# Performance work log

Hardware: AMD Instinct MI355X
Metric: run time of the kernel (lower is better)

## Reference

```python
import jax, jax.numpy as jnp
import numpy as np
from jax import lax

B, N, C = 256, 256, 192
HEADS = 6
HD = C // HEADS
WIN = 16
AGENT = 49
POOL = 7            # int(agent_num ** 0.5)
SCALE = HD ** -0.5


def _pool_matrix(inn, out):
    # PyTorch AdaptiveAvgPool2d bin edges: start=floor(i*inn/out), end=ceil((i+1)*inn/out)
    P = np.zeros((out, inn), np.float32)
    for i in range(out):
        s = (i * inn) // out
        e = -(((-(i + 1)) * inn) // out)
        P[i, s:e] = 1.0 / (e - s)
    return jnp.asarray(P)

_P = _pool_matrix(WIN, POOL)  # (7, 16) adaptive-avg-pool operator


def _resize_bilinear(x, out_h, out_w):
    # matches F.interpolate(mode='bilinear', align_corners=False)
    H, W = x.shape[-2], x.shape[-1]
    def idx(out, inn):
        s = (jnp.arange(out, dtype=jnp.float32) + 0.5) * (inn / out) - 0.5
        s = jnp.maximum(s, 0.0)
        i0 = jnp.minimum(jnp.floor(s).astype(jnp.int32), inn - 1)
        i1 = jnp.minimum(i0 + 1, inn - 1)
        return i0, i1, s - i0.astype(jnp.float32)
    h0, h1, th = idx(out_h, H)
    w0, w1, tw = idx(out_w, W)
    xh = x[..., h0, :] * (1.0 - th)[:, None] + x[..., h1, :] * th[:, None]
    return xh[..., :, w0] * (1.0 - tw) + xh[..., :, w1] * tw


def setup_inputs() -> dict:
    key = jax.random.key(0)
    ks = jax.random.split(key, 18)
    lin = lambda k: jax.random.normal(k, (C, C), jnp.float32) * 0.02
    zc = jnp.zeros((C,), jnp.float32)
    tn = lambda k, shp: jax.random.normal(k, shp, jnp.float32) * 0.02
    return {
        "x_F1": jax.random.normal(ks[0], (B, N, C), jnp.float32),
        "x_C2": jax.random.normal(ks[1], (B, N, C), jnp.float32),
        "x_C1": jax.random.normal(ks[2], (B, N, C), jnp.float32),
        "Wq": lin(ks[3]), "bq": zc,
        "Wk": lin(ks[4]), "bk": zc,
        "Wv": lin(ks[5]), "bv": zc,
        "Wa1": lin(ks[6]), "ba1": zc,
        "Wa2": lin(ks[7]), "ba2": zc,
        "an_bias": tn(ks[8], (HEADS, AGENT, 7, 7)),
        "na_bias": tn(ks[9], (HEADS, AGENT, 7, 7)),
        "ah_bias": tn(ks[10], (1, HEADS, AGENT, WIN, 1)),
        "aw_bias": tn(ks[11], (1, HEADS, AGENT, 1, WIN)),
        "ha_bias": tn(ks[12], (1, HEADS, WIN, 1, AGENT)),
        "wa_bias": tn(ks[13], (1, HEADS, 1, WIN, AGENT)),
        "dwc_w": tn(ks[14], (C, 1, 3, 3)),
        "dwc_b": zc,
        "Wp": lin(ks[15]), "bp": zc,
    }


def reference(x_F1, x_C2, x_C1, Wq, bq, Wk, bk, Wv, bv, Wa1, ba1, Wa2, ba2,
              an_bias, na_bias, ah_bias, aw_bias, ha_bias, wa_bias,
              dwc_w, dwc_b, Wp, bp):
    b, n, c = x_F1.shape
    h = w = WIN
    q = x_F1 @ Wq.T + bq
    k = (x_F1 + x_C2 - x_C1) @ Wk.T + bk
    v = (x_C2 - x_C1) @ Wv.T + bv
    # agent tokens: linear -> adaptive avg pool 16x16 -> 7x7 -> (b, 49, c)
    a1 = (x_C1 @ Wa1.T + ba1).reshape(b, h, w, c)
    a1 = jnp.einsum('ph,bhwc,qw->bpqc', _P, a1, _P).reshape(b, AGENT, c)
    a2 = (x_C2 @ Wa2.T + ba2).reshape(b, h, w, c)
    a2 = jnp.einsum('ph,bhwc,qw->bpqc', _P, a2, _P).reshape(b, AGENT, c)
    qh = q.reshape(b, n, HEADS, HD).transpose(0, 2, 1, 3)
    kh = k.reshape(b, n, HEADS, HD).transpose(0, 2, 1, 3)
    vh = v.reshape(b, n, HEADS, HD).transpose(0, 2, 1, 3)
    a1h = a1.reshape(b, AGENT, HEADS, HD).transpose(0, 2, 1, 3)
    a2h = a2.reshape(b, AGENT, HEADS, HD).transpose(0, 2, 1, 3)
    # stage 1: agent <- k/v attention, bias = interp(an_bias) + (ah+aw)
    pb = (_resize_bilinear(an_bias, h, w).reshape(1, HEADS, AGENT, n)
          + (ah_bias + aw_bias).reshape(1, HEADS, AGENT, n))
    attn2 = jax.nn.softmax(SCALE * jnp.einsum('bhad,bhnd->bhan', a2h, kh) + pb, axis=-1)
    agent_v = jnp.einsum('bhan,bhnd->bhad', attn2, vh)
    # stage 2: query <- agent attention, bias = interp(na_bias)^T + (ha+wa)
    ab = (jnp.swapaxes(_resize_bilinear(na_bias, h, w).reshape(HEADS, AGENT, n), -1, -2)[None]
          + (ha_bias + wa_bias).reshape(1, HEADS, n, AGENT))
    q_attn = jax.nn.softmax(SCALE * jnp.einsum('bhnd,bhad->bhna', qh, a1h) + ab, axis=-1)
    x = jnp.einsum('bhna,bhad->bhnd', q_attn, agent_v).transpose(0, 2, 1, 3).reshape(b, n, c)
    # depthwise 3x3 conv on q as spatial map
    q_img = q.reshape(b, h, w, c).transpose(0, 3, 1, 2)
    dw = lax.conv_general_dilated(q_img, dwc_w, (1, 1), ((1, 1), (1, 1)),
                                  feature_group_count=c,
                                  dimension_numbers=('NCHW', 'OIHW', 'NCHW'))
    dw = dw + dwc_b.reshape(1, c, 1, 1)
    x = x + dw.transpose(0, 2, 3, 1).reshape(b, n, c)
    return x @ Wp.T + bp
```

## Files before the change

### kernel.cpp

```cpp
#include <hip/hip_runtime.h>

typedef __bf16 bf16;
typedef __bf16 bf16x4 __attribute__((ext_vector_type(4)));
typedef __bf16 bf16x8 __attribute__((ext_vector_type(8)));
typedef float  f32x4  __attribute__((ext_vector_type(4)));

#define DEVI __device__ __forceinline__

static constexpr int   BATCH = 256;
static constexpr int   SEQ   = 256;
static constexpr int   CH    = 192;
static constexpr int   NH    = 6;
static constexpr int   AG    = 49;
static constexpr float QK_SCALE = 0.17677669529663687f;

__device__ constexpr int   PPN[16]  = {1,1,2,1,2,1,2,1,1,2,1,2,1,2,1,1};
__device__ constexpr int   PPB0[16] = {0,0,0,1,1,2,2,3,3,3,4,4,5,5,6,6};
__device__ constexpr int   PPB1[16] = {0,0,1,0,2,0,3,0,0,4,0,5,0,6,0,0};
__device__ constexpr float PPW0[16] = {1.f/3.f,1.f/3.f,1.f/3.f,1.f/3.f,1.f/3.f,1.f/3.f,1.f/3.f,0.25f,0.25f,0.25f,
                                       1.f/3.f,1.f/3.f,1.f/3.f,1.f/3.f,1.f/3.f,1.f/3.f};
__device__ constexpr float PPW1[16] = {0.f,0.f,1.f/3.f,0.f,1.f/3.f,0.f,0.25f,0.f,0.f,1.f/3.f,
                                       0.f,1.f/3.f,0.f,1.f/3.f,0.f,0.f};

#if defined(__has_builtin)
#if __has_builtin(__builtin_amdgcn_global_load_lds)
#define HAVE_GLL 1
#endif
#endif

DEVI void gll16(const void* g, void* l, int lane) {
#ifdef HAVE_GLL
  (void)lane;
  __builtin_amdgcn_global_load_lds(
      (const __attribute__((address_space(1))) void*)g,
      (__attribute__((address_space(3))) void*)l, 16, 0, 0);
#else
  *(uint4*)((char*)l + lane * 16) = *(const uint4*)((const char*)g);
#endif
}

DEVI float bilin7(const float* m, int i, int j) {
  float sh = (i + 0.5f) * 0.4375f - 0.5f; sh = sh < 0.f ? 0.f : sh;
  float sw = (j + 0.5f) * 0.4375f - 0.5f; sw = sw < 0.f ? 0.f : sw;
  int i0 = (int)sh; if (i0 > 6) i0 = 6;
  int j0 = (int)sw; if (j0 > 6) j0 = 6;
  int i1 = i0 + 1;  if (i1 > 6) i1 = 6;
  int j1 = j0 + 1;  if (j1 > 6) j1 = 6;
  float th = sh - (float)i0, tw = sw - (float)j0;
  float v00 = m[i0*7 + j0], v01 = m[i0*7 + j1];
  float v10 = m[i1*7 + j0], v11 = m[i1*7 + j1];
  return (v00*(1.f-tw) + v01*tw)*(1.f-th) + (v10*(1.f-tw) + v11*tw)*th;
}

__global__ void k_prep(const float* Wq, const float* Wk, const float* Wv,
                       const float* Wa1, const float* Wa2, const float* Wp,
                       const float* an_bias, const float* na_bias,
                       const float* ah_bias, const float* aw_bias,
                       const float* ha_bias, const float* wa_bias,
                       bf16* wsW, bf16* pb, bf16* ab, bf16* a1, bf16* a2) {
  int gid = blockIdx.x * 256 + threadIdx.x;
  if (gid < 221184) {
    int mi = gid / 36864, r = gid - mi * 36864;
    const float* W = (mi == 0 ? Wq : mi == 1 ? Wk : mi == 2 ? Wv :
                      mi == 3 ? Wa1 : mi == 4 ? Wa2 : Wp);
    wsW[gid] = (bf16)W[r];
  } else if (gid < 296448) {
    int r = gid - 221184;
    int n = r & 255, ha = r >> 8;
    int i = n >> 4, j = n & 15;
    float val = bilin7(an_bias + (size_t)ha * 49, i, j)
              + ah_bias[ha * 16 + i] + aw_bias[ha * 16 + j];
    pb[r] = (bf16)val;
  } else if (gid < 382464) {
    int r = gid - 296448;
    int a = r % 56, hn = r / 56;
    int n = hn & 255, hh = hn >> 8;
    int i = n >> 4, j = n & 15;
    float val = 0.f;
    if (a < AG)
      val = bilin7(na_bias + (size_t)(hh * 49 + a) * 49, i, j)
          + ha_bias[(hh * 16 + i) * 49 + a] + wa_bias[(hh * 16 + j) * 49 + a];
    ab[r] = (bf16)val;
  } else if (gid < 407040) {
    int r = gid - 382464;
    if (r < 12288) a1[(size_t)12544 * CH + r] = (bf16)0.f;
    else           a2[(size_t)12544 * CH + (r - 12288)] = (bf16)0.f;
  }
}

__global__ __launch_bounds__(256, 4) void k_combo(
    const float* xF1, const float* xC2, const float* xC1,
    bf16* f1b, bf16* kin, bf16* vin) {
  const int base = blockIdx.x * 1536 + threadIdx.x;
  #pragma unroll
  for (int g = 0; g < 2; ++g) {
    int rows[3], byts[3];
    float f[3][8], c2[3][8], c1[3][8];
    #pragma unroll
    for (int s = 0; s < 3; ++s) {
      const int slot = base + 256 * (3 * g + s);
      const int row  = slot / 24;
      const int cb   = slot - row * 24;
      rows[s] = row;
      byts[s] = (cb * 16) ^ ((row & 7) << 4);
      const size_t rf = (size_t)row * CH + cb * 8;
      *(float4*)&f[s][0]  = *(const float4*)(xF1 + rf);
      *(float4*)&f[s][4]  = *(const float4*)(xF1 + rf + 4);
      *(float4*)&c2[s][0] = *(const float4*)(xC2 + rf);
      *(float4*)&c2[s][4] = *(const float4*)(xC2 + rf + 4);
      *(float4*)&c1[s][0] = *(const float4*)(xC1 + rf);
      *(float4*)&c1[s][4] = *(const float4*)(xC1 + rf + 4);
    }
    #pragma unroll
    for (int s = 0; s < 3; ++s) {
      bf16x8 tq, tk, tv;
      #pragma unroll
      for (int e = 0; e < 8; ++e) {
        const float d = c2[s][e] - c1[s][e];
        tq[e] = (bf16)f[s][e];
        tk[e] = (bf16)(f[s][e] + d);
        tv[e] = (bf16)d;
      }
      const size_t rowb = (size_t)rows[s] * 384;
      *(bf16x8*)((char*)f1b + rowb + byts[s]) = tq;
      *(bf16x8*)((char*)kin + rowb + byts[s]) = tk;
      *(bf16x8*)((char*)vin + rowb + byts[s]) = tv;
    }
  }
}

__global__ __launch_bounds__(256, 3) void k_gemm3b(
    const bf16* f1b, const bf16* kin, const bf16* vin, const bf16* wsW,
    const float* bq, const float* bk, const float* bv,
    bf16* qO, bf16* kO, bf16* vO) {
  __shared__ char sA[49152] __attribute__((aligned(16)));
  const int tid = threadIdx.x, lane = tid & 63, wid = tid >> 6;
  const int l15 = lane & 15, lg = lane >> 4;
  const int wr = wid >> 1, wc = wid & 1;
  const int job = blockIdx.y;
  const int m0 = blockIdx.x * 128;
  const bf16*  Aj   = (job == 0 ? f1b : job == 1 ? kin : vin);
  const bf16*  Wj   = wsW + job * 36864;
  const float* bias = (job == 0 ? bq : job == 1 ? bk : bv);
  bf16*        outp = (job == 0 ? qO : job == 1 ? kO : vO);

  {
    const char* gsrc = (const char*)Aj + (size_t)m0 * 384;
    #pragma unroll
    for (int i = 0; i < 12; ++i) {
      const int off = (wid * 12 + i) * 1024;
      gll16(gsrc + off + lane * 16, sA + off, lane);
    }
  }
  __syncthreads();

  f32x4 acc[4][6];
  #pragma unroll
  for (int a = 0; a < 4; ++a)
    #pragma unroll
    for (int b2 = 0; b2 < 6; ++b2) acc[a][b2] = f32x4{0.f, 0.f, 0.f, 0.f};

  #pragma unroll
  for (int kk = 0; kk < 6; ++kk) {
    bf16x8 af[4];
    #pragma unroll
    for (int rt = 0; rt < 4; ++rt) {
      const int row = 64 * wr + 16 * rt + l15;
      af[rt] = *(const bf16x8*)(sA + row * 384 + ((kk * 64 + lg * 16) ^ ((row & 7) << 4)));
    }
    #pragma unroll
    for (int ct = 0; ct < 6; ++ct) {
      const int ncol = 96 * wc + 16 * ct + l15;
      bf16x8 bfr = *(const bf16x8*)&Wj[(size_t)ncol * CH + kk * 32 + 8 * lg];
      #pragma unroll
      for (int rt = 0; rt < 4; ++rt)
        acc[rt][ct] = __builtin_amdgcn_mfma_f32_16x16x32_bf16(af[rt], bfr, acc[rt][ct], 0, 0, 0);
    }
  }
  __syncthreads();
  #pragma unroll
  for (int ct = 0; ct < 6; ++ct) {
    const int col = 96 * wc + 16 * ct + l15;
    const float bb = bias[col];
    #pragma unroll
    for (int rt = 0; rt < 4; ++rt)
      #pragma unroll
      for (int r = 0; r < 4; ++r) {
        const int row = 64 * wr + 16 * rt + 4 * lg + r;
        *(bf16*)(sA + row * 384 + ((2 * col) ^ ((row & 7) << 4))) = (bf16)(acc[rt][ct][r] + bb);
      }
  }
  __syncthreads();
  #pragma unroll
  for (int g = 0; g < 12; ++g) {
    const int ch  = tid + 256 * g;
    const int row = ch / 24;
    const int y   = (ch - row * 24) * 16;
    bf16x8 vv = *(const bf16x8*)(sA + row * 384 + (y ^ ((row & 7) << 4)));
    *(bf16x8*)((char*)outp + (size_t)(m0 + row) * 384 + y) = vv;
  }
}

#define POOLROW(I, P0, W0, P1, W1) do {                                        \
    float jqx[7] = {0,0,0,0,0,0,0}, jqy[7] = {0,0,0,0,0,0,0};                  \
    _Pragma("unroll")                                                          \
    for (int j = 0; j < 16; ++j) {                                             \
      float2 x = *(const float2*)(src + (size_t)((I) * 16 + j) * CH);          \
      jqx[PPB0[j]] += PPW0[j] * x.x;  jqy[PPB0[j]] += PPW0[j] * x.y;           \
      if (PPN[j] == 2) { jqx[PPB1[j]] += PPW1[j] * x.x;                        \
                         jqy[PPB1[j]] += PPW1[j] * x.y; }                      \
    }                                                                          \
    _Pragma("unroll")                                                          \
    for (int q = 0; q < 7; ++q) { ax[P0][q] += (W0) * jqx[q];                  \
                                  ay[P0][q] += (W0) * jqy[q]; }                \
    if ((P1) >= 0) {                                                           \
      _Pragma("unroll")                                                        \
      for (int q = 0; q < 7; ++q) { ax[(P1) & 3][q] += (W1) * jqx[q];          \
                                    ay[(P1) & 3][q] += (W1) * jqy[q]; }        \
    }                                                                          \
  } while (0)

__global__ __launch_bounds__(192) void k_pool(
    const float* xC1, const float* xC2, bf16* pooled1, bf16* pooled2) {
  __shared__ float lred[7][192];
  const int b = blockIdx.x, which = blockIdx.y, t = threadIdx.x;
  const int cp = t % 96, ih = t / 96;
  const float* src = (which ? xC2 : xC1) + (size_t)b * SEQ * CH + 2 * cp;
  bf16* dst = (which ? pooled2 : pooled1) + (size_t)b * AG * CH + 2 * cp;

  float ax[4][7], ay[4][7];
  #pragma unroll
  for (int p = 0; p < 4; ++p)
    #pragma unroll
    for (int q = 0; q < 7; ++q) { ax[p][q] = 0.f; ay[p][q] = 0.f; }

  const float TH = 1.f / 3.f, QU = 0.25f;
  if (ih == 0) {
    POOLROW(0, 0, TH, -1, 0.f);  POOLROW(1, 0, TH, -1, 0.f);
    POOLROW(2, 0, TH,  1, TH);   POOLROW(3, 1, TH, -1, 0.f);
    POOLROW(4, 1, TH,  2, TH);   POOLROW(5, 2, TH, -1, 0.f);
    POOLROW(6, 2, TH,  3, QU);   POOLROW(7, 3, QU, -1, 0.f);
  } else {
    POOLROW(8,  0, QU, -1, 0.f); POOLROW(9,  0, QU,  1, TH);
    POOLROW(10, 1, TH, -1, 0.f); POOLROW(11, 1, TH,  2, TH);
    POOLROW(12, 2, TH, -1, 0.f); POOLROW(13, 2, TH,  3, TH);
    POOLROW(14, 3, TH, -1, 0.f); POOLROW(15, 3, TH, -1, 0.f);
  }
  if (ih == 1) {
    #pragma unroll
    for (int q = 0; q < 7; ++q) {
      lred[q][2 * cp] = ax[0][q]; lred[q][2 * cp + 1] = ay[0][q];
    }
  }
  __syncthreads();
  if (ih == 0) {
    #pragma unroll
    for (int q = 0; q < 7; ++q) {
      ax[3][q] += lred[q][2 * cp]; ay[3][q] += lred[q][2 * cp + 1];
    }
    #pragma unroll
    for (int p = 0; p < 4; ++p)
      #pragma unroll
      for (int q = 0; q < 7; ++q) {
        union { bf16 e[2]; unsigned u; } u;
        u.e[0] = (bf16)ax[p][q]; u.e[1] = (bf16)ay[p][q];
        *(unsigned*)&dst[(size_t)(p * 7 + q) * CH] = u.u;
      }
  } else {
    #pragma unroll
    for (int lp = 1; lp < 4; ++lp)
      #pragma unroll
      for (int q = 0; q < 7; ++q) {
        union { bf16 e[2]; unsigned u; } u;
        u.e[0] = (bf16)ax[lp][q]; u.e[1] = (bf16)ay[lp][q];
        *(unsigned*)&dst[(size_t)((3 + lp) * 7 + q) * CH] = u.u;
      }
  }
}

DEVI void gemm_body(const bf16* Asrc, const bf16* W, const float* bias,
                    bf16* outp, int m0, bf16 (*sA)[72]) {
  const int tid = threadIdx.x, lane = tid & 63, wid = tid >> 6;
  const int l15 = lane & 15, lg = lane >> 4;
  const int wr = wid >> 1, wc = wid & 1;
  const int srow = tid >> 1, shalf = tid & 1;

  f32x4 acc[4][6];
  #pragma unroll
  for (int a = 0; a < 4; ++a)
    #pragma unroll
    for (int b2 = 0; b2 < 6; ++b2) acc[a][b2] = f32x4{0.f, 0.f, 0.f, 0.f};

  for (int ks = 0; ks < 3; ++ks) {
    const int k0 = ks * 64;
    const uint4* src = (const uint4*)(Asrc + (size_t)(m0 + srow) * CH + k0 + shalf * 32);
    #pragma unroll
    for (int i2 = 0; i2 < 4; ++i2)
      *(uint4*)&sA[srow][shalf * 32 + 8 * i2] = src[i2];
    __syncthreads();
    #pragma unroll
    for (int kk = 0; kk < 64; kk += 32) {
      bf16x8 af[4];
      #pragma unroll
      for (int rt = 0; rt < 4; ++rt)
        af[rt] = *(const bf16x8*)&sA[64 * wr + 16 * rt + l15][kk + 8 * lg];
      #pragma unroll
      for (int ct = 0; ct < 6; ++ct) {
        const int ncol = 96 * wc + 16 * ct + l15;
        bf16x8 bfr = *(const bf16x8*)&W[(size_t)ncol * CH + k0 + kk + 8 * lg];
        #pragma unroll
        for (int rt = 0; rt < 4; ++rt)
          acc[rt][ct] = __builtin_amdgcn_mfma_f32_16x16x32_bf16(af[rt], bfr, acc[rt][ct], 0, 0, 0);
      }
    }
    __syncthreads();
  }
  #pragma unroll
  for (int ct = 0; ct < 6; ++ct) {
    const int col = 96 * wc + 16 * ct + l15;
    const float bb = bias[col];
    #pragma unroll
    for (int rt = 0; rt < 4; ++rt) {
      const size_t rbase = (size_t)(m0 + 64 * wr + 16 * rt + 4 * lg);
      #pragma unroll
      for (int r = 0; r < 4; ++r)
        outp[(rbase + r) * CH + col] = (bf16)(acc[rt][ct][r] + bb);
    }
  }
}

__global__ __launch_bounds__(256, 2) void k_gemm2(
    const bf16* pooled1, const bf16* pooled2, const bf16* wsW,
    const float* ba1, const float* ba2, bf16* a1, bf16* a2) {
  __shared__ bf16 sA[128][72] __attribute__((aligned(16)));
  const int m0 = blockIdx.x * 128;
  if (blockIdx.y == 0) gemm_body(pooled1, wsW + 3 * 36864, ba1, a1, m0, sA);
  else                 gemm_body(pooled2, wsW + 4 * 36864, ba2, a2, m0, sA);
}

__global__ __launch_bounds__(256, 3) void k_gemm_out(
    const bf16* xsum, const bf16* Wp, const float* bp, float* out) {
  __shared__ char sA[49152] __attribute__((aligned(16)));
  const int tid = threadIdx.x, lane = tid & 63, wid = tid >> 6;
  const int l15 = lane & 15, lg = lane >> 4;
  const int wr = wid >> 1, wc = wid & 1;
  const int m0 = blockIdx.x * 128;

  {
    const char* gsrc = (const char*)xsum + (size_t)m0 * 384;
    #pragma unroll
    for (int i = 0; i < 12; ++i) {
      const int off = (wid * 12 + i) * 1024;
      gll16(gsrc + off + lane * 16, sA + off, lane);
    }
  }
  __syncthreads();

  f32x4 acc[4][6];
  #pragma unroll
  for (int a = 0; a < 4; ++a)
    #pragma unroll
    for (int b2 = 0; b2 < 6; ++b2) acc[a][b2] = f32x4{0.f, 0.f, 0.f, 0.f};

  #pragma unroll
  for (int kk = 0; kk < 6; ++kk) {
    bf16x8 af[4];
    #pragma unroll
    for (int rt = 0; rt < 4; ++rt) {
      const int row = 64 * wr + 16 * rt + l15;
      af[rt] = *(const bf16x8*)(sA + row * 384 + ((kk * 64 + lg * 16) ^ ((row & 7) << 4)));
    }
    #pragma unroll
    for (int ct = 0; ct < 6; ++ct) {
      const int ncol = 96 * wc + 16 * ct + l15;
      bf16x8 bfr = *(const bf16x8*)&Wp[(size_t)ncol * CH + kk * 32 + 8 * lg];
      #pragma unroll
      for (int rt = 0; rt < 4; ++rt)
        acc[rt][ct] = __builtin_amdgcn_mfma_f32_16x16x32_bf16(af[rt], bfr, acc[rt][ct], 0, 0, 0);
    }
  }
  #pragma unroll
  for (int ct = 0; ct < 6; ++ct) {
    const int col = 96 * wc + 16 * ct + l15;
    const float bb = bp[col];
    #pragma unroll
    for (int rt = 0; rt < 4; ++rt)
      #pragma unroll
      for (int r = 0; r < 4; ++r)
        out[(size_t)(m0 + 64 * wr + 16 * rt + 4 * lg + r) * CH + col] = acc[rt][ct][r] + bb;
  }
}

__global__ __launch_bounds__(256, 2) void k_attn(
    const bf16* q, const bf16* k, const bf16* v,
    const bf16* a1, const bf16* a2, const bf16* pb, const bf16* ab,
    const float* dwc_w, const float* dwc_b, bf16* xsum) {
  const int h = blockIdx.x, b = blockIdx.y;
  __shared__ char uSmem[36864] __attribute__((aligned(16)));
  bf16 (*log1)[264] = reinterpret_cast<bf16 (*)[264]>(uSmem);
  bf16 (*log2)[72]  = reinterpret_cast<bf16 (*)[72]>(uSmem);
  __shared__ bf16 sVT[32][264] __attribute__((aligned(16)));
  __shared__ bf16 sAVT[32][72] __attribute__((aligned(16)));
  __shared__ float srow1[64];
  __shared__ float srow2[256];
  __shared__ bf16 xat[256][36] __attribute__((aligned(16)));
  __shared__ float sW[9][32];
  __shared__ float dwb[32];

  const int tid = threadIdx.x, lane = tid & 63, wv = tid >> 6;
  const int l15 = lane & 15, lg = lane >> 4;

  const bf16* qb  = q  + (size_t)b * SEQ * CH + h * 32;
  const bf16* kb  = k  + (size_t)b * SEQ * CH + h * 32;
  const bf16* vb  = v  + (size_t)b * SEQ * CH + h * 32;
  const bf16* a1b = a1 + (size_t)b * AG  * CH + h * 32;
  const bf16* a2b = a2 + (size_t)b * AG  * CH + h * 32;

  for (int idx = tid; idx < 288; idx += 256) {
    const int cl = idx / 9, tap = idx - cl * 9;
    sW[tap][cl] = dwc_w[(32 * h + cl) * 9 + tap];
  }
  if (tid < 32) dwb[tid] = dwc_b[32 * h + tid];

  {
    const int p = tid & 127, dg = tid >> 7;
    const bf16* s0 = vb + (size_t)(2 * p) * CH + dg * 16;
    bf16x8 r0a = ((const bf16x8*)s0)[0];
    bf16x8 r0b = ((const bf16x8*)s0)[1];
    bf16x8 r1a = ((const bf16x8*)(s0 + CH))[0];
    bf16x8 r1b = ((const bf16x8*)(s0 + CH))[1];
    #pragma unroll
    for (int j = 0; j < 8; ++j) {
      union { bf16 e[2]; unsigned u; } u0, u1;
      u0.e[0] = r0a[j]; u0.e[1] = r1a[j];
      u1.e[0] = r0b[j]; u1.e[1] = r1b[j];
      *(unsigned*)&sVT[dg * 16 + j][2 * p]     = u0.u;
      *(unsigned*)&sVT[dg * 16 + 8 + j][2 * p] = u1.u;
    }
  }

  {
    bf16x8 afr[4];
    #pragma unroll
    for (int rt = 0; rt < 4; ++rt)
      afr[rt] = *(const bf16x8*)(a2b + (size_t)(16 * rt + l15) * CH + 8 * lg);
    #pragma unroll
    for (int ct = 0; ct < 4; ++ct) {
      const int n = 64 * wv + 16 * ct + l15;
      bf16x8 bfr = *(const bf16x8*)(kb + (size_t)n * CH + 8 * lg);
      #pragma unroll
      for (int rt = 0; rt < 4; ++rt) {
        f32x4 acc = {0.f, 0.f, 0.f, 0.f};
        acc = __builtin_amdgcn_mfma_f32_16x16x32_bf16(afr[rt], bfr, acc, 0, 0, 0);
        #pragma unroll
        for (int r = 0; r < 4; ++r)
          log1[16 * rt + 4 * lg + r][n] = (bf16)acc[r];
      }
    }
  }
  __syncthreads();

  if (tid < 196) {
    const int a = tid >> 2, qu = tid & 3;
    const bf16* pbrow = pb + ((size_t)h * AG + a) * SEQ + qu * 64;
    float vbuf[64];
    float m = -1e30f;
    #pragma unroll
    for (int i2 = 0; i2 < 8; ++i2) {
      bf16x8 raw = *(const bf16x8*)&log1[a][qu * 64 + 8 * i2];
      bf16x8 pbb = *(const bf16x8*)&pbrow[8 * i2];
      #pragma unroll
      for (int j = 0; j < 8; ++j) {
        float x = QK_SCALE * (float)raw[j] + (float)pbb[j];
        vbuf[8 * i2 + j] = x;
        m = fmaxf(m, x);
      }
    }
    m = fmaxf(m, __shfl_xor(m, 1));
    m = fmaxf(m, __shfl_xor(m, 2));
    float s = 0.f;
    #pragma unroll
    for (int i2 = 0; i2 < 8; ++i2) {
      bf16x8 eb;
      #pragma unroll
      for (int j = 0; j < 8; ++j) {
        float e = __expf(vbuf[8 * i2 + j] - m);
        s += e;
        eb[j] = (bf16)e;
      }
      *(bf16x8*)&log1[a][qu * 64 + 8 * i2] = eb;
    }
    s += __shfl_xor(s, 1);
    s += __shfl_xor(s, 2);
    if (qu == 0) srow1[a] = 1.f / s;
  }
  __syncthreads();

  {
    f32x4 acc0 = {0.f, 0.f, 0.f, 0.f}, acc1 = {0.f, 0.f, 0.f, 0.f};
    #pragma unroll
    for (int ksn = 0; ksn < 8; ++ksn) {
      bf16x8 af = *(const bf16x8*)&log1[16 * wv + l15][32 * ksn + 8 * lg];
      bf16x8 b0 = *(const bf16x8*)&sVT[l15][32 * ksn + 8 * lg];
      bf16x8 b1 = *(const bf16x8*)&sVT[16 + l15][32 * ksn + 8 * lg];
      acc0 = __builtin_amdgcn_mfma_f32_16x16x32_bf16(af, b0, acc0, 0, 0, 0);
      acc1 = __builtin_amdgcn_mfma_f32_16x16x32_bf16(af, b1, acc1, 0, 0, 0);
    }
    #pragma unroll
    for (int r = 0; r < 4; ++r) {
      const int a = 16 * wv + 4 * lg + r;
      const float inv = (a < AG) ? srow1[a] : 0.f;
      sAVT[l15][a]      = (bf16)(acc0[r] * inv);
      sAVT[16 + l15][a] = (bf16)(acc1[r] * inv);
    }
  }
  __syncthreads();

  {
    bf16x8 bfr[4];
    #pragma unroll
    for (int ct = 0; ct < 4; ++ct)
      bfr[ct] = *(const bf16x8*)(a1b + (size_t)(16 * ct + l15) * CH + 8 * lg);
    #pragma unroll
    for (int rt = 0; rt < 4; ++rt) {
      bf16x8 af = *(const bf16x8*)(qb + (size_t)(64 * wv + 16 * rt + l15) * CH + 8 * lg);
      #pragma unroll
      for (int ct = 0; ct < 4; ++ct) {
        f32x4 acc = {0.f, 0.f, 0.f, 0.f};
        acc = __builtin_amdgcn_mfma_f32_16x16x32_bf16(af, bfr[ct], acc, 0, 0, 0);
        #pragma unroll
        for (int r = 0; r < 4; ++r)
          log2[64 * wv + 16 * rt + 4 * lg + r][16 * ct + l15] = (bf16)acc[r];
      }
    }
  }
  __syncthreads();

  {
    const bf16* abrow = ab + ((size_t)h * SEQ + tid) * 56;
    float vb2[49];
    float m = -1e30f;
    #pragma unroll
    for (int i2 = 0; i2 < 6; ++i2) {
      bf16x8 raw = *(const bf16x8*)&log2[tid][8 * i2];
      bf16x8 abb = *(const bf16x8*)&abrow[8 * i2];
      #pragma unroll
      for (int j = 0; j < 8; ++j) {
        float x = QK_SCALE * (float)raw[j] + (float)abb[j];
        vb2[8 * i2 + j] = x;
        m = fmaxf(m, x);
      }
    }
    {
      float x = QK_SCALE * (float)log2[tid][48] + (float)abrow[48];
      vb2[48] = x;
      m = fmaxf(m, x);
    }
    float s = 0.f;
    #pragma unroll
    for (int i2 = 0; i2 < 8; ++i2) {
      bf16x8 eb;
      #pragma unroll
      for (int j = 0; j < 8; ++j) {
        const int idx = 8 * i2 + j;
        float e = 0.f;
        if (idx < AG) { e = __expf(vb2[idx] - m); }
        s += e;
        eb[j] = (bf16)e;
      }
      *(bf16x8*)&log2[tid][8 * i2] = eb;
    }
    srow2[tid] = 1.f / s;
  }
  __syncthreads();

  {
    bf16x8 bfr[2][2];
    #pragma unroll
    for (int ksn = 0; ksn < 2; ++ksn) {
      bfr[ksn][0] = *(const bf16x8*)&sAVT[l15][32 * ksn + 8 * lg];
      bfr[ksn][1] = *(const bf16x8*)&sAVT[16 + l15][32 * ksn + 8 * lg];
    }
    #pragma unroll
    for (int rt = 0; rt < 4; ++rt) {
      f32x4 acc0 = {0.f, 0.f, 0.f, 0.f}, acc1 = {0.f, 0.f, 0.f, 0.f};
      #pragma unroll
      for (int ksn = 0; ksn < 2; ++ksn) {
        bf16x8 af = *(const bf16x8*)&log2[64 * wv + 16 * rt + l15][32 * ksn + 8 * lg];
        acc0 = __builtin_amdgcn_mfma_f32_16x16x32_bf16(af, bfr[ksn][0], acc0, 0, 0, 0);
        acc1 = __builtin_amdgcn_mfma_f32_16x16x32_bf16(af, bfr[ksn][1], acc1, 0, 0, 0);
      }
      #pragma unroll
      for (int r = 0; r < 4; ++r) {
        const int nq = 64 * wv + 16 * rt + 4 * lg + r;
        const float inv = srow2[nq];
        xat[nq][l15]      = (bf16)(acc0[r] * inv);
        xat[nq][16 + l15] = (bf16)(acc1[r] * inv);
      }
    }
  }
  __syncthreads();

  {
    const int n = tid, ii = n >> 4, jj = n & 15;
    float acc[32];
    #pragma unroll
    for (int u = 0; u < 4; ++u) {
      bf16x4 xa0 = *(const bf16x4*)&xat[n][8 * u];
      bf16x4 xa1 = *(const bf16x4*)&xat[n][8 * u + 4];
      #pragma unroll
      for (int e = 0; e < 4; ++e) {
        acc[8 * u + e]     = dwb[8 * u + e]     + (float)xa0[e];
        acc[8 * u + 4 + e] = dwb[8 * u + 4 + e] + (float)xa1[e];
      }
    }
    #pragma unroll
    for (int di = 0; di < 3; ++di) {
      const int i2 = ii + di - 1;
      if ((unsigned)i2 >= 16u) continue;
      #pragma unroll
      for (int dj = 0; dj < 3; ++dj) {
        const int j2 = jj + dj - 1;
        if ((unsigned)j2 >= 16u) continue;
        const int tap = di * 3 + dj;
        const bf16* qr = q + ((size_t)b * SEQ + i2 * 16 + j2) * CH + h * 32;
        #pragma unroll
        for (int u = 0; u < 4; ++u) {
          bf16x8 qv = *(const bf16x8*)(qr + 8 * u);
          const float4* wv4 = (const float4*)&sW[tap][8 * u];
          float4 wa = wv4[0], wb2 = wv4[1];
          acc[8*u+0] += (float)qv[0] * wa.x;  acc[8*u+1] += (float)qv[1] * wa.y;
          acc[8*u+2] += (float)qv[2] * wa.z;  acc[8*u+3] += (float)qv[3] * wa.w;
          acc[8*u+4] += (float)qv[4] * wb2.x; acc[8*u+5] += (float)qv[5] * wb2.y;
          acc[8*u+6] += (float)qv[6] * wb2.z; acc[8*u+7] += (float)qv[7] * wb2.w;
        }
      }
    }
    char* xo = (char*)xsum + (size_t)(b * SEQ + n) * 384;
    const int sw = (n & 7) << 4;
    #pragma unroll
    for (int u = 0; u < 4; ++u) {
      bf16x8 ob;
      #pragma unroll
      for (int e = 0; e < 8; ++e) ob[e] = (bf16)acc[8 * u + e];
      *(bf16x8*)(xo + ((64 * h + 16 * u) ^ sw)) = ob;
    }
  }
}

extern "C" void kernel_launch(void* const* d_in, const int* in_sizes, int n_in,
                              void* d_out, int out_size, void* d_ws, size_t ws_size,
                              hipStream_t stream) {
  (void)in_sizes; (void)n_in; (void)out_size; (void)ws_size;
  const float* xF1 = (const float*)d_in[0];
  const float* xC2 = (const float*)d_in[1];
  const float* xC1 = (const float*)d_in[2];
  const float* Wq  = (const float*)d_in[3];
  const float* bq  = (const float*)d_in[4];
  const float* Wk  = (const float*)d_in[5];
  const float* bk  = (const float*)d_in[6];
  const float* Wv  = (const float*)d_in[7];
  const float* bv  = (const float*)d_in[8];
  const float* Wa1 = (const float*)d_in[9];
  const float* ba1 = (const float*)d_in[10];
  const float* Wa2 = (const float*)d_in[11];
  const float* ba2 = (const float*)d_in[12];
  const float* an_bias = (const float*)d_in[13];
  const float* na_bias = (const float*)d_in[14];
  const float* ah_bias = (const float*)d_in[15];
  const float* aw_bias = (const float*)d_in[16];
  const float* ha_bias = (const float*)d_in[17];
  const float* wa_bias = (const float*)d_in[18];
  const float* dwc_w = (const float*)d_in[19];
  const float* dwc_b = (const float*)d_in[20];
  const float* Wp  = (const float*)d_in[21];
  const float* bp  = (const float*)d_in[22];

  char* ws = (char*)d_ws;
  size_t off = 0;
  auto nxt = [&](size_t bytes) -> char* {
    char* p = ws + off;
    off = (off + bytes + 255) & ~(size_t)255;
    return p;
  };
  const size_t XSZ = (size_t)BATCH * SEQ * CH;
  const size_t ASZ = ((size_t)BATCH * AG + 64) * CH;

  bf16*  wsW     = (bf16*)nxt(6 * 36864 * sizeof(bf16));
  bf16*  pb      = (bf16*)nxt(6 * 49 * 256 * sizeof(bf16));
  bf16*  ab      = (bf16*)nxt(6 * 256 * 56 * sizeof(bf16));
  bf16*  pooled1 = (bf16*)nxt(ASZ * sizeof(bf16));
  bf16*  pooled2 = (bf16*)nxt(ASZ * sizeof(bf16));
  bf16*  f1b     = (bf16*)nxt(XSZ * sizeof(bf16));
  bf16*  kin     = (bf16*)nxt(XSZ * sizeof(bf16));
  bf16*  vin     = (bf16*)nxt(XSZ * sizeof(bf16));
  bf16*  qB      = (bf16*)nxt(XSZ * sizeof(bf16));
  bf16*  kB      = (bf16*)nxt(XSZ * sizeof(bf16));
  bf16*  vB      = (bf16*)nxt(XSZ * sizeof(bf16));
  bf16*  a1B     = (bf16*)nxt(ASZ * sizeof(bf16));
  bf16*  a2B     = (bf16*)nxt(ASZ * sizeof(bf16));
  bf16*  xsum    = kin;

  k_prep<<<1590, 256, 0, stream>>>(Wq, Wk, Wv, Wa1, Wa2, Wp,
                                   an_bias, na_bias, ah_bias, aw_bias,
                                   ha_bias, wa_bias, wsW, pb, ab, a1B, a2B);
  k_combo<<<1024, 256, 0, stream>>>(xF1, xC2, xC1, f1b, kin, vin);
  k_gemm3b<<<dim3(512, 3), 256, 0, stream>>>(f1b, kin, vin, wsW, bq, bk, bv, qB, kB, vB);
  k_pool<<<dim3(BATCH, 2), 192, 0, stream>>>(xC1, xC2, pooled1, pooled2);
  k_gemm2<<<dim3(98, 2), 256, 0, stream>>>(pooled1, pooled2, wsW, ba1, ba2, a1B, a2B);
  k_attn<<<dim3(NH, BATCH), 256, 0, stream>>>(qB, kB, vB, a1B, a2B, pb, ab,
                                              dwc_w, dwc_b, xsum);
  k_gemm_out<<<512, 256, 0, stream>>>(xsum, wsW + 5 * 36864, bp, (float*)d_out);
}
```

Before: 230.0 us.

## Emit V transposed from projection GEMM and shrink attention shared memory

The V projection epilogue now writes V in a per-(batch, head) transposed layout, so the attention kernel reads its MFMA B operands straight from global memory and no longer stages a transpose through shared memory. Shared buffers in the attention kernel are packed into one union with a narrower log2 row and fewer padded writes. Launch bounds rise from 2 to 3 blocks per CU to allow more occupancy. In exchange, the attention kernel does strided global reads of V for each k-step instead of shared-memory reads, and the GEMM epilogue gains a transposed scatter.

```diff
diff --git a/kernel.cpp b/kernel.cpp
--- a/kernel.cpp
+++ b/kernel.cpp
@@ -132,7 +132,7 @@
 __global__ __launch_bounds__(256, 3) void k_gemm3b(
     const bf16* f1b, const bf16* kin, const bf16* vin, const bf16* wsW,
     const float* bq, const float* bk, const float* bv,
-    bf16* qO, bf16* kO, bf16* vO) {
+    bf16* qO, bf16* kO, bf16* vT) {
   __shared__ char sA[49152] __attribute__((aligned(16)));
   const int tid = threadIdx.x, lane = tid & 63, wid = tid >> 6;
   const int l15 = lane & 15, lg = lane >> 4;
@@ -142,7 +142,6 @@
   const bf16*  Aj   = (job == 0 ? f1b : job == 1 ? kin : vin);
   const bf16*  Wj   = wsW + job * 36864;
   const float* bias = (job == 0 ? bq : job == 1 ? bk : bv);
-  bf16*        outp = (job == 0 ? qO : job == 1 ? kO : vO);
 
   {
     const char* gsrc = (const char*)Aj + (size_t)m0 * 384;
@@ -178,26 +177,53 @@
     }
   }
   __syncthreads();
-  #pragma unroll
-  for (int ct = 0; ct < 6; ++ct) {
-    const int col = 96 * wc + 16 * ct + l15;
-    const float bb = bias[col];
-    #pragma unroll
-    for (int rt = 0; rt < 4; ++rt)
-      #pragma unroll
-      for (int r = 0; r < 4; ++r) {
-        const int row = 64 * wr + 16 * rt + 4 * lg + r;
-        *(bf16*)(sA + row * 384 + ((2 * col) ^ ((row & 7) << 4))) = (bf16)(acc[rt][ct][r] + bb);
-      }
-  }
-  __syncthreads();
-  #pragma unroll
-  for (int g = 0; g < 12; ++g) {
-    const int ch  = tid + 256 * g;
-    const int row = ch / 24;
-    const int y   = (ch - row * 24) * 16;
-    bf16x8 vv = *(const bf16x8*)(sA + row * 384 + (y ^ ((row & 7) << 4)));
-    *(bf16x8*)((char*)outp + (size_t)(m0 + row) * 384 + y) = vv;
+
+  if (job < 2) {
+    bf16* outp = (job == 0 ? qO : kO);
+    #pragma unroll
+    for (int ct = 0; ct < 6; ++ct) {
+      const int col = 96 * wc + 16 * ct + l15;
+      const float bb = bias[col];
+      #pragma unroll
+      for (int rt = 0; rt < 4; ++rt)
+        #pragma unroll
+        for (int r = 0; r < 4; ++r) {
+          const int row = 64 * wr + 16 * rt + 4 * lg + r;
+          *(bf16*)(sA + row * 384 + ((2 * col) ^ ((row & 7) << 4))) = (bf16)(acc[rt][ct][r] + bb);
+        }
+    }
+    __syncthreads();
+    #pragma unroll
+    for (int g = 0; g < 12; ++g) {
+      const int ch  = tid + 256 * g;
+      const int row = ch / 24;
+      const int y   = (ch - row * 24) * 16;
+      bf16x8 vv = *(const bf16x8*)(sA + row * 384 + (y ^ ((row & 7) << 4)));
+      *(bf16x8*)((char*)outp + (size_t)(m0 + row) * 384 + y) = vv;
+    }
+  } else {
+    #pragma unroll
+    for (int ct = 0; ct < 6; ++ct) {
+      const int col = 96 * wc + 16 * ct + l15;
+      const float bb = bias[col];
+      #pragma unroll
+      for (int rt = 0; rt < 4; ++rt)
+        #pragma unroll
+        for (int r = 0; r < 4; ++r) {
+          const int row = 64 * wr + 16 * rt + 4 * lg + r;
+          const int byt = col * 256 + (((2 * row) & ~15) ^ ((col & 7) << 4)) + ((2 * row) & 15);
+          *(bf16*)(sA + byt) = (bf16)(acc[rt][ct][r] + bb);
+        }
+    }
+    __syncthreads();
+    const int batch = m0 >> 8, nb = m0 & 255;
+    #pragma unroll
+    for (int g = 0; g < 12; ++g) {
+      const int ch = tid + 256 * g;
+      const int c = ch >> 4, o = ch & 15;
+      bf16x8 vv = *(const bf16x8*)(sA + c * 256 + ((o * 16) ^ ((c & 7) << 4)));
+      *(bf16x8*)(vT + (((size_t)batch * NH + (c >> 5)) * 32 + (c & 31)) * 256 + nb + 8 * o) = vv;
+    }
   }
 }
 
@@ -391,28 +417,27 @@
   }
 }
 
-__global__ __launch_bounds__(256, 2) void k_attn(
-    const bf16* q, const bf16* k, const bf16* v,
+__global__ __launch_bounds__(256, 3) void k_attn(
+    const bf16* q, const bf16* k, const bf16* vT,
     const bf16* a1, const bf16* a2, const bf16* pb, const bf16* ab,
     const float* dwc_w, const float* dwc_b, bf16* xsum) {
   const int h = blockIdx.x, b = blockIdx.y;
-  __shared__ char uSmem[36864] __attribute__((aligned(16)));
-  bf16 (*log1)[264] = reinterpret_cast<bf16 (*)[264]>(uSmem);
-  bf16 (*log2)[72]  = reinterpret_cast<bf16 (*)[72]>(uSmem);
-  __shared__ bf16 sVT[32][264] __attribute__((aligned(16)));
-  __shared__ bf16 sAVT[32][72] __attribute__((aligned(16)));
+  __shared__ char U[51712] __attribute__((aligned(16)));
   __shared__ float srow1[64];
   __shared__ float srow2[256];
-  __shared__ bf16 xat[256][36] __attribute__((aligned(16)));
   __shared__ float sW[9][32];
   __shared__ float dwb[32];
+  bf16 (*log1)[264] = reinterpret_cast<bf16 (*)[264]>(U);
+  bf16 (*log2)[56]  = reinterpret_cast<bf16 (*)[56]>(U);
+  bf16 (*xat)[36]   = reinterpret_cast<bf16 (*)[36]>(U + 28672);
+  bf16 (*sAVT)[72]  = reinterpret_cast<bf16 (*)[72]>(U + 47104);
 
   const int tid = threadIdx.x, lane = tid & 63, wv = tid >> 6;
   const int l15 = lane & 15, lg = lane >> 4;
 
   const bf16* qb  = q  + (size_t)b * SEQ * CH + h * 32;
   const bf16* kb  = k  + (size_t)b * SEQ * CH + h * 32;
-  const bf16* vb  = v  + (size_t)b * SEQ * CH + h * 32;
+  const bf16* vTb = vT + ((size_t)(b * NH + h) * 32) * 256;
   const bf16* a1b = a1 + (size_t)b * AG  * CH + h * 32;
   const bf16* a2b = a2 + (size_t)b * AG  * CH + h * 32;
 
@@ -421,23 +446,6 @@
     sW[tap][cl] = dwc_w[(32 * h + cl) * 9 + tap];
   }
   if (tid < 32) dwb[tid] = dwc_b[32 * h + tid];
-
-  {
-    const int p = tid & 127, dg = tid >> 7;
-    const bf16* s0 = vb + (size_t)(2 * p) * CH + dg * 16;
-    bf16x8 r0a = ((const bf16x8*)s0)[0];
-    bf16x8 r0b = ((const bf16x8*)s0)[1];
-    bf16x8 r1a = ((const bf16x8*)(s0 + CH))[0];
-    bf16x8 r1b = ((const bf16x8*)(s0 + CH))[1];
-    #pragma unroll
-    for (int j = 0; j < 8; ++j) {
-      union { bf16 e[2]; unsigned u; } u0, u1;
-      u0.e[0] = r0a[j]; u0.e[1] = r1a[j];
-      u1.e[0] = r0b[j]; u1.e[1] = r1b[j];
-      *(unsigned*)&sVT[dg * 16 + j][2 * p]     = u0.u;
-      *(unsigned*)&sVT[dg * 16 + 8 + j][2 * p] = u1.u;
-    }
-  }
 
   {
     bf16x8 afr[4];
@@ -501,8 +509,8 @@
     #pragma unroll
     for (int ksn = 0; ksn < 8; ++ksn) {
       bf16x8 af = *(const bf16x8*)&log1[16 * wv + l15][32 * ksn + 8 * lg];
-      bf16x8 b0 = *(const bf16x8*)&sVT[l15][32 * ksn + 8 * lg];
-      bf16x8 b1 = *(const bf16x8*)&sVT[16 + l15][32 * ksn + 8 * lg];
+      bf16x8 b0 = *(const bf16x8*)(vTb + (size_t)l15 * 256 + 32 * ksn + 8 * lg);
+      bf16x8 b1 = *(const bf16x8*)(vTb + (size_t)(16 + l15) * 256 + 32 * ksn + 8 * lg);
       acc0 = __builtin_amdgcn_mfma_f32_16x16x32_bf16(af, b0, acc0, 0, 0, 0);
       acc1 = __builtin_amdgcn_mfma_f32_16x16x32_bf16(af, b1, acc1, 0, 0, 0);
     }
@@ -528,9 +536,11 @@
       for (int ct = 0; ct < 4; ++ct) {
         f32x4 acc = {0.f, 0.f, 0.f, 0.f};
         acc = __builtin_amdgcn_mfma_f32_16x16x32_bf16(af, bfr[ct], acc, 0, 0, 0);
-        #pragma unroll
-        for (int r = 0; r < 4; ++r)
-          log2[64 * wv + 16 * rt + 4 * lg + r][16 * ct + l15] = (bf16)acc[r];
+        if (ct < 3 || l15 == 0) {
+          #pragma unroll
+          for (int r = 0; r < 4; ++r)
+            log2[64 * wv + 16 * rt + 4 * lg + r][16 * ct + l15] = (bf16)acc[r];
+        }
       }
     }
   }
@@ -558,7 +568,7 @@
     }
     float s = 0.f;
     #pragma unroll
-    for (int i2 = 0; i2 < 8; ++i2) {
+    for (int i2 = 0; i2 < 7; ++i2) {
       bf16x8 eb;
       #pragma unroll
       for (int j = 0; j < 8; ++j) {
@@ -696,7 +706,7 @@
   bf16*  vin     = (bf16*)nxt(XSZ * sizeof(bf16));
   bf16*  qB      = (bf16*)nxt(XSZ * sizeof(bf16));
   bf16*  kB      = (bf16*)nxt(XSZ * sizeof(bf16));
-  bf16*  vB      = (bf16*)nxt(XSZ * sizeof(bf16));
+  bf16*  vTB     = (bf16*)nxt(XSZ * sizeof(bf16));
   bf16*  a1B     = (bf16*)nxt(ASZ * sizeof(bf16));
   bf16*  a2B     = (bf16*)nxt(ASZ * sizeof(bf16));
   bf16*  xsum    = kin;
@@ -705,10 +715,10 @@
                                    an_bias, na_bias, ah_bias, aw_bias,
                                    ha_bias, wa_bias, wsW, pb, ab, a1B, a2B);
   k_combo<<<1024, 256, 0, stream>>>(xF1, xC2, xC1, f1b, kin, vin);
-  k_gemm3b<<<dim3(512, 3), 256, 0, stream>>>(f1b, kin, vin, wsW, bq, bk, bv, qB, kB, vB);
+  k_gemm3b<<<dim3(512, 3), 256, 0, stream>>>(f1b, kin, vin, wsW, bq, bk, bv, qB, kB, vTB);
   k_pool<<<dim3(BATCH, 2), 192, 0, stream>>>(xC1, xC2, pooled1, pooled2);
   k_gemm2<<<dim3(98, 2), 256, 0, stream>>>(pooled1, pooled2, wsW, ba1, ba2, a1B, a2B);
-  k_attn<<<dim3(NH, BATCH), 256, 0, stream>>>(qB, kB, vB, a1B, a2B, pb, ab,
+  k_attn<<<dim3(NH, BATCH), 256, 0, stream>>>(qB, kB, vTB, a1B, a2B, pb, ab,
                                               dwc_w, dwc_b, xsum);
   k_gemm_out<<<512, 256, 0, stream>>>(xsum, wsW + 5 * 36864, bp, (float*)d_out);
 }
```

After: 232.2 us. About the same (+1.0%).
